# Kernel optimization log

Hardware: AMD Instinct MI355X
Metric: run time of the kernel (lower is better)

## Reference

```python
import jax, jax.numpy as jnp
import numpy as np

N_NODES = 50000
N_EDGES = 800000
IN_DIM = 512
HIDDEN = 512
NUM_HASH = 4
HASH_DIM = 128
NUM_GRAPHS = 64
NUM_CLASSES = 10


def _hash_mats(rng, num_hash, in_dim, hash_dim):
    # Each row of each hash matrix has a single +-1 entry at a random column.
    cols = rng.integers(0, hash_dim, size=(num_hash, in_dim))
    signs = (rng.integers(0, 2, size=(num_hash, in_dim)) * 2 - 1).astype(np.float32)
    W = np.zeros((num_hash, in_dim, hash_dim), dtype=np.float32)
    W[np.arange(num_hash)[:, None], np.arange(in_dim)[None, :], cols] = signs
    return jnp.asarray(W)


def setup_inputs() -> dict:
    key = jax.random.key(0)
    ks = jax.random.split(key, 10)
    rng = np.random.default_rng(0)
    x = jax.random.normal(ks[0], (N_NODES, IN_DIM), dtype=jnp.float32)
    edge_index = jax.random.randint(ks[1], (2, N_EDGES), 0, N_NODES, dtype=jnp.int64)
    batch = jnp.sort(jax.random.randint(ks[2], (N_NODES,), 0, NUM_GRAPHS, dtype=jnp.int64))
    s1 = 1.0 / np.sqrt(NUM_HASH * HASH_DIM)
    s2 = 1.0 / np.sqrt(IN_DIM)
    s3 = 1.0 / np.sqrt(HIDDEN)
    return {
        "x": x,
        "edge_index": edge_index,
        "batch": batch,
        "Hm1": _hash_mats(rng, NUM_HASH, IN_DIM, HASH_DIM),
        "Wp1": jax.random.normal(ks[3], (NUM_HASH * HASH_DIM, HIDDEN), dtype=jnp.float32) * s1,
        "Ws1": jax.random.normal(ks[4], (IN_DIM, HIDDEN), dtype=jnp.float32) * s2,
        "b1": jnp.zeros((HIDDEN,), dtype=jnp.float32),
        "Hm2": _hash_mats(rng, NUM_HASH, HIDDEN, HASH_DIM),
        "Wp2": jax.random.normal(ks[5], (NUM_HASH * HASH_DIM, HIDDEN), dtype=jnp.float32) * s1,
        "Ws2": jax.random.normal(ks[6], (HIDDEN, HIDDEN), dtype=jnp.float32) * s3,
        "b2": jnp.zeros((HIDDEN,), dtype=jnp.float32),
        "Wc": jax.random.normal(ks[7], (HIDDEN, NUM_CLASSES), dtype=jnp.float32) * s3,
        "bc": jnp.zeros((NUM_CLASSES,), dtype=jnp.float32),
    }


def _demo_layer(h, src, dst, deg, Hm, Wp, Ws, b):
    n = h.shape[0]
    # Degree-bucketed gather + mean == segment-mean over edges by source node.
    nsum = jax.ops.segment_sum(h[dst], src, num_segments=n)  # [N, D]
    agg = jnp.where(deg[:, None] > 0, nsum / jnp.maximum(deg, 1.0)[:, None], h)
    # Multi-hash matmul + concat: [N, K*HASH_DIM]
    hashed = jnp.einsum("nd,kdh->nkh", agg, Hm).reshape(n, -1)
    out = hashed @ Wp + h @ Ws + b
    return jax.nn.elu(out)  # dropout is identity in eval mode


def reference(x, edge_index, batch, Hm1, Wp1, Ws1, b1, Hm2, Wp2, Ws2, b2, Wc, bc):
    n = x.shape[0]
    src, dst = edge_index[0], edge_index[1]
    deg = jax.ops.segment_sum(jnp.ones(src.shape, x.dtype), src, num_segments=n)
    h = _demo_layer(x, src, dst, deg, Hm1, Wp1, Ws1, b1)
    h = _demo_layer(h, src, dst, deg, Hm2, Wp2, Ws2, b2)
    # global mean pool per graph
    cnt = jax.ops.segment_sum(jnp.ones((n,), h.dtype), batch, num_segments=NUM_GRAPHS)
    g = jax.ops.segment_sum(h, batch, num_segments=NUM_GRAPHS) / jnp.maximum(cnt, 1.0)[:, None]
    return g @ Wc + bc
```

## Files before the change

kernel.cpp:

```cpp
#include <hip/hip_runtime.h>
#include <hip/hip_bf16.h>
#include <math.h>

#define N_NODES_C 50000
#define N_EDGES_C 800000
#define DIM 512
#define NUM_GRAPHS_C 64
#define NUM_CLASSES_C 10

#define NROWT ((N_NODES_C + 127) / 128)
#define GEMM_BLOCKS (((NROWT * 4 + 31) / 32) * 32)

#define SCAN_BLK 1024
#define SCAN_NBLK ((N_NODES_C + SCAN_BLK - 1) / SCAN_BLK)

typedef short bf16x8 __attribute__((ext_vector_type(8)));
typedef short bf16x4 __attribute__((ext_vector_type(4)));
typedef float f32x4 __attribute__((ext_vector_type(4)));
typedef float f32x2 __attribute__((ext_vector_type(2)));
typedef unsigned u32x2 __attribute__((ext_vector_type(2)));

__device__ __forceinline__ float bf2f(short s) {
    return __uint_as_float(((unsigned)(unsigned short)s) << 16);
}
__device__ __forceinline__ short f2bf(float f) {
    unsigned u = __float_as_uint(f);
    u += 0x7FFF + ((u >> 16) & 1);
    return (short)(u >> 16);
}
__device__ __forceinline__ float eluf(float v) {
    return v > 0.0f ? v : __expf(v) - 1.0f;
}
__device__ __forceinline__ unsigned f32x4_to_fp8(float a, float b, float c, float d) {
    int w = 0;
    w = __builtin_amdgcn_cvt_pk_fp8_f32(a, b, w, false);
    w = __builtin_amdgcn_cvt_pk_fp8_f32(c, d, w, true);
    return (unsigned)w;
}
__device__ __forceinline__ void acc_fp8x8(float* acc, u32x2 w) {
    f32x2 a = __builtin_amdgcn_cvt_pk_f32_fp8((int)w[0], false);
    f32x2 b = __builtin_amdgcn_cvt_pk_f32_fp8((int)w[0], true);
    f32x2 c = __builtin_amdgcn_cvt_pk_f32_fp8((int)w[1], false);
    f32x2 d = __builtin_amdgcn_cvt_pk_f32_fp8((int)w[1], true);
    acc[0] += a[0]; acc[1] += a[1]; acc[2] += b[0]; acc[3] += b[1];
    acc[4] += c[0]; acc[5] += c[1]; acc[6] += d[0]; acc[7] += d[1];
}

__device__ __forceinline__ void gl16(const void* g, void* l) {
    __builtin_amdgcn_global_load_lds(
        (const __attribute__((address_space(1))) unsigned*)g,
        (__attribute__((address_space(3))) unsigned*)l, 16, 0, 0);
}


__global__ void k_hist(const int* __restrict__ src, int* __restrict__ cnt) {
    int e = blockIdx.x * blockDim.x + threadIdx.x;
    if (e < N_EDGES_C) atomicAdd(&cnt[src[e]], 1);
}

__global__ __launch_bounds__(1024)
void k_bsum(const int* __restrict__ cnt, int* __restrict__ bsum) {
    __shared__ int sh[1024];
    int i = blockIdx.x * 1024 + threadIdx.x;
    sh[threadIdx.x] = (i < N_NODES_C) ? cnt[i] : 0;
    __syncthreads();
    for (int ofs = 512; ofs > 0; ofs >>= 1) {
        if ((int)threadIdx.x < ofs) sh[threadIdx.x] += sh[threadIdx.x + ofs];
        __syncthreads();
    }
    if (threadIdx.x == 0) bsum[blockIdx.x] = sh[0];
}

__global__ __launch_bounds__(64)
void k_bscan(const int* __restrict__ bsum, int* __restrict__ bofs,
             int* __restrict__ start) {
    int l = threadIdx.x;
    int own = (l < SCAN_NBLK) ? bsum[l] : 0;
    int v = own;
    for (int ofs = 1; ofs < 64; ofs <<= 1) {
        int t = __shfl_up(v, ofs, 64);
        if (l >= ofs) v += t;
    }
    if (l < SCAN_NBLK) bofs[l] = v - own;
    if (l == 63) start[N_NODES_C] = v;
}

__global__ __launch_bounds__(1024)
void k_scan_apply(const int* __restrict__ cnt, const int* __restrict__ bofs,
                  int* __restrict__ start, int* __restrict__ cursor) {
    __shared__ int sh[1024];
    int i = blockIdx.x * 1024 + threadIdx.x;
    int v = (i < N_NODES_C) ? cnt[i] : 0;
    sh[threadIdx.x] = v;
    __syncthreads();
    for (int ofs = 1; ofs < 1024; ofs <<= 1) {
        int t = (threadIdx.x >= (unsigned)ofs) ? sh[threadIdx.x - ofs] : 0;
        __syncthreads();
        sh[threadIdx.x] += t;
        __syncthreads();
    }
    if (i < N_NODES_C) {
        int ex = bofs[blockIdx.x] + sh[threadIdx.x] - v;
        start[i] = ex;
        cursor[i] = ex;
    }
}

__global__ void k_fill(const int* __restrict__ src, const int* __restrict__ dst,
                       int* __restrict__ cursor, int* __restrict__ ebuf) {
    int e = blockIdx.x * blockDim.x + threadIdx.x;
    if (e < N_EDGES_C) {
        int pos = atomicAdd(&cursor[src[e]], 1);
        ebuf[pos] = dst[e];
    }
}

__global__ __launch_bounds__(1024)
void k_cnt(const int* __restrict__ batch, int* __restrict__ cnt) {
    __shared__ int h[NUM_GRAPHS_C];
    if (threadIdx.x < NUM_GRAPHS_C) h[threadIdx.x] = 0;
    __syncthreads();
    int n = blockIdx.x * blockDim.x + threadIdx.x;
    if (n < N_NODES_C) {
        int g = batch[n];
        if ((unsigned)g < NUM_GRAPHS_C) atomicAdd(&h[g], 1);
    }
    __syncthreads();
    if (threadIdx.x < NUM_GRAPHS_C && h[threadIdx.x] > 0)
        atomicAdd(&cnt[threadIdx.x], h[threadIdx.x]);
}

__global__ void k_weff(const float* __restrict__ Hm, const float* __restrict__ Wp,
                       float* __restrict__ Weff) {
    __shared__ int   scol[4];
    __shared__ float ssign[4];
    int d = blockIdx.x;
    int h = threadIdx.x;
    for (int k = 0; k < 4; ++k) {
        float v = Hm[((size_t)k * DIM + d) * 128 + h];
        if (v != 0.0f) { scol[k] = h; ssign[k] = v; }
    }
    __syncthreads();
    for (int j = threadIdx.x; j < DIM; j += 128) {
        float acc = 0.0f;
#pragma unroll
        for (int k = 0; k < 4; ++k)
            acc += ssign[k] * Wp[(size_t)(k * 128 + scol[k]) * DIM + j];
        Weff[(size_t)d * DIM + j] = acc;
    }
}

__global__ void k_prepw(const float* __restrict__ Weff, const float* __restrict__ Ws,
                        short* __restrict__ Wt) {
    int n = blockIdx.x;
    for (int k = threadIdx.x; k < 2 * DIM; k += 256) {
        float v = (k < DIM) ? Weff[(size_t)k * DIM + n] : Ws[(size_t)(k - DIM) * DIM + n];
        Wt[(size_t)n * (2 * DIM) + k] = f2bf(v);
    }
}

__global__ void k_cast(const float* __restrict__ x, short* __restrict__ xb,
                       unsigned char* __restrict__ xq) {
    int idx = blockIdx.x * blockDim.x + threadIdx.x;
    if (idx >= N_NODES_C * DIM / 8) return;
    const float* p = x + (size_t)idx * 8;
    float v[8];
    bf16x8 o;
#pragma unroll
    for (int j = 0; j < 8; ++j) { v[j] = p[j]; o[j] = f2bf(v[j]); }
    u32x2 q;
    q[0] = f32x4_to_fp8(v[0], v[1], v[2], v[3]);
    q[1] = f32x4_to_fp8(v[4], v[5], v[6], v[7]);
    *(bf16x8*)(xb + (size_t)idx * 8) = o;
    *(u32x2*)(xq + (size_t)idx * 8) = q;
}

__global__ __launch_bounds__(256)
void k_gather_8(const unsigned char* __restrict__ Hq, const int* __restrict__ start,
                const int* __restrict__ ebuf, const short* __restrict__ fb,
                short* __restrict__ outb) {
    int n = blockIdx.x * 4 + (threadIdx.x >> 6);
    int l = threadIdx.x & 63;
    if (n >= N_NODES_C) return;
    int s = start[n], e = start[n + 1];
    float acc[8] = {0, 0, 0, 0, 0, 0, 0, 0};
    int i = s;
    if (i + 4 <= e) {
        int d0 = ebuf[i], d1 = ebuf[i + 1], d2 = ebuf[i + 2], d3 = ebuf[i + 3];
        for (; i + 8 <= e; i += 4) {
            int n0 = ebuf[i + 4], n1 = ebuf[i + 5], n2 = ebuf[i + 6], n3 = ebuf[i + 7];
            u32x2 w0 = *(const u32x2*)(Hq + (size_t)d0 * DIM + l * 8);
            u32x2 w1 = *(const u32x2*)(Hq + (size_t)d1 * DIM + l * 8);
            u32x2 w2 = *(const u32x2*)(Hq + (size_t)d2 * DIM + l * 8);
            u32x2 w3 = *(const u32x2*)(Hq + (size_t)d3 * DIM + l * 8);
            acc_fp8x8(acc, w0); acc_fp8x8(acc, w1);
            acc_fp8x8(acc, w2); acc_fp8x8(acc, w3);
            d0 = n0; d1 = n1; d2 = n2; d3 = n3;
        }
        {
            u32x2 w0 = *(const u32x2*)(Hq + (size_t)d0 * DIM + l * 8);
            u32x2 w1 = *(const u32x2*)(Hq + (size_t)d1 * DIM + l * 8);
            u32x2 w2 = *(const u32x2*)(Hq + (size_t)d2 * DIM + l * 8);
            u32x2 w3 = *(const u32x2*)(Hq + (size_t)d3 * DIM + l * 8);
            acc_fp8x8(acc, w0); acc_fp8x8(acc, w1);
            acc_fp8x8(acc, w2); acc_fp8x8(acc, w3);
            i += 4;
        }
    }
    for (; i < e; ++i) {
        int d0 = ebuf[i];
        u32x2 w0 = *(const u32x2*)(Hq + (size_t)d0 * DIM + l * 8);
        acc_fp8x8(acc, w0);
    }
    bf16x8 o;
    if (e > s) {
        float inv = 1.0f / (float)(e - s);
#pragma unroll
        for (int j = 0; j < 8; ++j) o[j] = f2bf(acc[j] * inv);
    } else {
        o = *(const bf16x8*)(fb + (size_t)n * DIM + l * 8);
    }
    *(bf16x8*)(outb + (size_t)n * DIM + l * 8) = o;
}


__device__ __forceinline__ void gemm_core(const short* __restrict__ A1,
                                          const short* __restrict__ A2,
                                          const short* __restrict__ Wt,
                                          short* As, short* Bs,
                                          int row0, int col0,
                                          int wave, int lane, f32x4 (*acc)[4]) {
    const int wm = wave >> 1, wn = wave & 1;
    const int q = lane >> 4, t16 = lane & 15;
    const int rloc = wave * 32 + (lane >> 3);
    const int csrc = (lane & 7) ^ (lane >> 3);
    size_t aoff[4], boff[4];
#pragma unroll
    for (int j = 0; j < 4; ++j) {
        int grow = row0 + rloc + j * 8;
        if (grow >= N_NODES_C) grow = N_NODES_C - 1;
        aoff[j] = (size_t)grow * DIM + csrc * 8;
        boff[j] = (size_t)(col0 + rloc + j * 8) * (2 * DIM) + csrc * 8;
    }
    short* AsW = As + wave * 2048;
    short* BsW = Bs + wave * 2048;
#pragma unroll
    for (int p = 0; p < 2; ++p) {
        const short* A = p ? A2 : A1;
        const short* W = Wt + p * DIM;
        for (int kt = 0; kt < DIM; kt += 64) {
            __syncthreads();
#pragma unroll
            for (int j = 0; j < 4; ++j) {
                gl16(A + aoff[j] + kt, AsW + j * 512);
                gl16(W + boff[j] + kt, BsW + j * 512);
            }
            __syncthreads();
#pragma unroll
            for (int kh = 0; kh < 2; ++kh) {
                bf16x8 af[4], bfv[4];
#pragma unroll
                for (int mi = 0; mi < 4; ++mi) {
                    int r = wm * 64 + mi * 16 + t16;
                    int cp = (kh * 4 + q) ^ (t16 & 7);
                    af[mi] = *(const bf16x8*)(As + r * 64 + cp * 8);
                }
#pragma unroll
                for (int ni = 0; ni < 4; ++ni) {
                    int r = wn * 64 + ni * 16 + t16;
                    int cp = (kh * 4 + q) ^ (t16 & 7);
                    bfv[ni] = *(const bf16x8*)(Bs + r * 64 + cp * 8);
                }
#pragma unroll
                for (int mi = 0; mi < 4; ++mi)
#pragma unroll
                    for (int ni = 0; ni < 4; ++ni)
                        acc[mi][ni] = __builtin_amdgcn_mfma_f32_16x16x32_bf16(
                            bfv[ni], af[mi], acc[mi][ni], 0, 0, 0);
            }
        }
    }
}

__global__ __launch_bounds__(256, 4)
void k_gemm_elu_mfma(const short* __restrict__ A1, const short* __restrict__ A2,
                     const short* __restrict__ Wt, const float* __restrict__ bias,
                     short* __restrict__ C, unsigned char* __restrict__ C8) {
    __shared__ __align__(16) short As[128 * 64];
    __shared__ __align__(16) short Bs[128 * 64];
    const int L = blockIdx.x;
    const int ct = (L & 31) >> 3;
    const int rt = ((L >> 5) << 3) + (L & 7);
    if (rt >= NROWT) return;
    const int row0 = rt * 128, col0 = ct * 128;
    const int tid = threadIdx.x;
    const int lane = tid & 63, wave = tid >> 6;
    const int wm = wave >> 1, wn = wave & 1;
    const int q = lane >> 4, t16 = lane & 15;
    f32x4 acc[4][4] = {};
    gemm_core(A1, A2, Wt, As, Bs, row0, col0, wave, lane, acc);
    f32x4 bv[4];
#pragma unroll
    for (int ni = 0; ni < 4; ++ni)
        bv[ni] = *(const f32x4*)(bias + col0 + wn * 64 + ni * 16 + q * 4);
#pragma unroll
    for (int mi = 0; mi < 4; ++mi) {
        int row = row0 + wm * 64 + mi * 16 + t16;
        if (row < N_NODES_C) {
#pragma unroll
            for (int ni = 0; ni < 4; ++ni) {
                int colq = col0 + wn * 64 + ni * 16 + q * 4;
                float v0 = eluf(acc[mi][ni][0] + bv[ni][0]);
                float v1 = eluf(acc[mi][ni][1] + bv[ni][1]);
                float v2 = eluf(acc[mi][ni][2] + bv[ni][2]);
                float v3 = eluf(acc[mi][ni][3] + bv[ni][3]);
                bf16x4 ob;
                ob[0] = f2bf(v0); ob[1] = f2bf(v1);
                ob[2] = f2bf(v2); ob[3] = f2bf(v3);
                *(bf16x4*)(C + (size_t)row * DIM + colq) = ob;
                *(unsigned*)(C8 + (size_t)row * DIM + colq) =
                    f32x4_to_fp8(v0, v1, v2, v3);
            }
        }
    }
}

__global__ __launch_bounds__(256, 4)
void k_gemm_pool_mfma(const short* __restrict__ A1, const short* __restrict__ A2,
                      const short* __restrict__ Wt, const float* __restrict__ bias,
                      const int* __restrict__ batch, float* __restrict__ gsum) {
    __shared__ __align__(16) short As[128 * 64];
    __shared__ __align__(16) short Bs[128 * 64];
    __shared__ int sbatch[128];
    const int L = blockIdx.x;
    const int ct = (L & 31) >> 3;
    const int rt = ((L >> 5) << 3) + (L & 7);
    if (rt >= NROWT) return;
    const int row0 = rt * 128, col0 = ct * 128;
    const int tid = threadIdx.x;
    const int lane = tid & 63, wave = tid >> 6;
    const int wm = wave >> 1, wn = wave & 1;
    const int q = lane >> 4, t16 = lane & 15;
    if (tid < 128) {
        int rw = row0 + tid;
        sbatch[tid] = (rw < N_NODES_C) ? batch[rw] : -1;
    }
    f32x4 acc[4][4] = {};
    gemm_core(A1, A2, Wt, As, Bs, row0, col0, wave, lane, acc);
    f32x4 bv[4];
#pragma unroll
    for (int ni = 0; ni < 4; ++ni)
        bv[ni] = *(const f32x4*)(bias + col0 + wn * 64 + ni * 16 + q * 4);
    const int g0 = sbatch[wm * 64];
    const int g63 = sbatch[wm * 64 + 63];
    if (g0 == g63) {
        if (g0 >= 0) {
#pragma unroll
            for (int ni = 0; ni < 4; ++ni) {
#pragma unroll
                for (int r = 0; r < 4; ++r) {
                    float s = 0.0f;
#pragma unroll
                    for (int mi = 0; mi < 4; ++mi)
                        s += eluf(acc[mi][ni][r] + bv[ni][r]);
                    s += __shfl_xor(s, 1, 64);
                    s += __shfl_xor(s, 2, 64);
                    s += __shfl_xor(s, 4, 64);
                    s += __shfl_xor(s, 8, 64);
                    if (t16 == 0)
                        atomicAdd(&gsum[(size_t)g0 * DIM + col0 + wn * 64 +
                                        ni * 16 + q * 4 + r], s);
                }
            }
        }
    } else if (g0 >= 0) {
        int g_th[4];
#pragma unroll
        for (int mi = 0; mi < 4; ++mi) g_th[mi] = sbatch[wm * 64 + mi * 16 + t16];
        int gmx = g0;
#pragma unroll
        for (int mi = 0; mi < 4; ++mi) gmx = max(gmx, g_th[mi]);
        gmx = max(gmx, __shfl_xor(gmx, 1, 64));
        gmx = max(gmx, __shfl_xor(gmx, 2, 64));
        gmx = max(gmx, __shfl_xor(gmx, 4, 64));
        gmx = max(gmx, __shfl_xor(gmx, 8, 64));
        for (int gsel = g0; gsel <= gmx; ++gsel) {
#pragma unroll
            for (int ni = 0; ni < 4; ++ni) {
#pragma unroll
                for (int r = 0; r < 4; ++r) {
                    float s = 0.0f;
#pragma unroll
                    for (int mi = 0; mi < 4; ++mi) {
                        float v = eluf(acc[mi][ni][r] + bv[ni][r]);
                        s += (g_th[mi] == gsel) ? v : 0.0f;
                    }
                    s += __shfl_xor(s, 1, 64);
                    s += __shfl_xor(s, 2, 64);
                    s += __shfl_xor(s, 4, 64);
                    s += __shfl_xor(s, 8, 64);
                    if (t16 == 0)
                        atomicAdd(&gsum[(size_t)gsel * DIM + col0 + wn * 64 +
                                        ni * 16 + q * 4 + r], s);
                }
            }
        }
    }
}

__global__ void k_final(const float* __restrict__ gsum, const int* __restrict__ cnt,
                        const float* __restrict__ Wc, const float* __restrict__ bc,
                        float* __restrict__ out) {
    int g = blockIdx.x;
    int j = threadIdx.x;
    if (j >= NUM_CLASSES_C) return;
    int c_ = cnt[g];
    float inv = 1.0f / (float)(c_ > 1 ? c_ : 1);
    float s = 0.0f;
    for (int c = 0; c < DIM; ++c)
        s += gsum[(size_t)g * DIM + c] * Wc[(size_t)c * NUM_CLASSES_C + j];
    out[g * NUM_CLASSES_C + j] = s * inv + bc[j];
}


extern "C" void kernel_launch(void* const* d_in, const int* in_sizes, int n_in,
                              void* d_out, int out_size, void* d_ws, size_t ws_size,
                              hipStream_t stream) {
    const float* x   = (const float*)d_in[0];
    const int*   ei  = (const int*)d_in[1];
    const int*   src = ei;
    const int*   dst = ei + N_EDGES_C;
    const int* batch = (const int*)d_in[2];
    const float* Hm1 = (const float*)d_in[3];
    const float* Wp1 = (const float*)d_in[4];
    const float* Ws1 = (const float*)d_in[5];
    const float* b1  = (const float*)d_in[6];
    const float* Hm2 = (const float*)d_in[7];
    const float* Wp2 = (const float*)d_in[8];
    const float* Ws2 = (const float*)d_in[9];
    const float* b2  = (const float*)d_in[10];
    const float* Wc  = (const float*)d_in[11];
    const float* bc  = (const float*)d_in[12];
    float* out = (float*)d_out;

    char* ws = (char*)d_ws;
    size_t off = 0;
    auto alloc = [&](size_t bytes) {
        void* p = ws + off;
        off += (bytes + 255) & ~(size_t)255;
        return p;
    };
    const size_t nodeB16 = (size_t)N_NODES_C * DIM * 2;
    const size_t nodeB8  = (size_t)N_NODES_C * DIM;
    short* xb    = (short*)alloc(nodeB16);
    short* aggB  = (short*)alloc(nodeB16);
    short* hB    = (short*)alloc(nodeB16);
    unsigned char* xq = (unsigned char*)alloc(nodeB8);
    unsigned char* hq = (unsigned char*)alloc(nodeB8);
    float* Weff1 = (float*)alloc((size_t)DIM * DIM * 4);
    float* Weff2 = (float*)alloc((size_t)DIM * DIM * 4);
    short* Wt1   = (short*)alloc((size_t)DIM * 2 * DIM * 2);
    short* Wt2   = (short*)alloc((size_t)DIM * 2 * DIM * 2);
    int*   cnt_i = (int*)alloc((size_t)N_NODES_C * 4);
    int*   start = (int*)alloc((size_t)(N_NODES_C + 1) * 4);
    int*   cursor= (int*)alloc((size_t)N_NODES_C * 4);
    int*   ebuf  = (int*)alloc((size_t)N_EDGES_C * 4);
    int*   cnt   = (int*)alloc((size_t)NUM_GRAPHS_C * 4);
    float* gsum  = (float*)alloc((size_t)NUM_GRAPHS_C * DIM * 4);
    int*   bsum  = (int*)alloc((size_t)SCAN_NBLK * 4);
    int*   bofs  = (int*)alloc((size_t)SCAN_NBLK * 4);

    hipMemsetAsync(cnt_i, 0, (size_t)N_NODES_C * 4, stream);
    hipMemsetAsync(cnt, 0, (size_t)NUM_GRAPHS_C * 4, stream);
    hipMemsetAsync(gsum, 0, (size_t)NUM_GRAPHS_C * DIM * 4, stream);

    k_hist<<<(N_EDGES_C + 255) / 256, 256, 0, stream>>>(src, cnt_i);
    k_bsum<<<SCAN_NBLK, 1024, 0, stream>>>(cnt_i, bsum);
    k_bscan<<<1, 64, 0, stream>>>(bsum, bofs, start);
    k_scan_apply<<<SCAN_NBLK, 1024, 0, stream>>>(cnt_i, bofs, start, cursor);
    k_fill<<<(N_EDGES_C + 255) / 256, 256, 0, stream>>>(src, dst, cursor, ebuf);
    k_cnt<<<(N_NODES_C + 1023) / 1024, 1024, 0, stream>>>(batch, cnt);
    k_weff<<<DIM, 128, 0, stream>>>(Hm1, Wp1, Weff1);
    k_weff<<<DIM, 128, 0, stream>>>(Hm2, Wp2, Weff2);
    k_prepw<<<DIM, 256, 0, stream>>>(Weff1, Ws1, Wt1);
    k_prepw<<<DIM, 256, 0, stream>>>(Weff2, Ws2, Wt2);
    k_cast<<<(N_NODES_C * DIM / 8 + 255) / 256, 256, 0, stream>>>(x, xb, xq);

    k_gather_8<<<(N_NODES_C + 3) / 4, 256, 0, stream>>>(xq, start, ebuf, xb, aggB);
    k_gemm_elu_mfma<<<GEMM_BLOCKS, 256, 0, stream>>>(aggB, xb, Wt1, b1, hB, hq);

    k_gather_8<<<(N_NODES_C + 3) / 4, 256, 0, stream>>>(hq, start, ebuf, hB, aggB);
    k_gemm_pool_mfma<<<GEMM_BLOCKS, 256, 0, stream>>>(aggB, hB, Wt2, b2, batch, gsum);

    k_final<<<NUM_GRAPHS_C, 64, 0, stream>>>(gsum, cnt, Wc, bc, out);
}
```

Measured before the change: 606.2 us.

## Merge scan and graph-count kernels, raise GEMM occupancy, drop batch LDS staging

Folds the per-graph node count into the block-sum kernel and the single-block offset scan into the scan-apply kernel, which removes two kernel launches. Both MFMA GEMM kernels now request 5 blocks per SM instead of 4, which may force tighter register allocation. The pooling GEMM reads batch ids straight from global memory instead of staging them in shared memory. In k_scan_apply, bofs_s is written by the first wave and read after the existing __syncthreads, so ordering is kept.

Result: slower. 776.5 us (+28.1%).

```diff
diff --git a/kernel.cpp b/kernel.cpp
--- a/kernel.cpp
+++ b/kernel.cpp
@@ -59,36 +59,44 @@
 }
 
 __global__ __launch_bounds__(1024)
-void k_bsum(const int* __restrict__ cnt, int* __restrict__ bsum) {
+void k_bsum(const int* __restrict__ cnt, int* __restrict__ bsum,
+            const int* __restrict__ batch, int* __restrict__ gcnt) {
     __shared__ int sh[1024];
+    __shared__ int h[NUM_GRAPHS_C];
+    if (threadIdx.x < NUM_GRAPHS_C) h[threadIdx.x] = 0;
     int i = blockIdx.x * 1024 + threadIdx.x;
-    sh[threadIdx.x] = (i < N_NODES_C) ? cnt[i] : 0;
+    int inb = (i < N_NODES_C);
+    sh[threadIdx.x] = inb ? cnt[i] : 0;
+    if (inb) {
+        int g = batch[i];
+        if ((unsigned)g < NUM_GRAPHS_C) atomicAdd(&h[g], 1);
+    }
     __syncthreads();
     for (int ofs = 512; ofs > 0; ofs >>= 1) {
         if ((int)threadIdx.x < ofs) sh[threadIdx.x] += sh[threadIdx.x + ofs];
         __syncthreads();
     }
     if (threadIdx.x == 0) bsum[blockIdx.x] = sh[0];
-}
-
-__global__ __launch_bounds__(64)
-void k_bscan(const int* __restrict__ bsum, int* __restrict__ bofs,
-             int* __restrict__ start) {
-    int l = threadIdx.x;
-    int own = (l < SCAN_NBLK) ? bsum[l] : 0;
-    int v = own;
-    for (int ofs = 1; ofs < 64; ofs <<= 1) {
-        int t = __shfl_up(v, ofs, 64);
-        if (l >= ofs) v += t;
-    }
-    if (l < SCAN_NBLK) bofs[l] = v - own;
-    if (l == 63) start[N_NODES_C] = v;
+    if (threadIdx.x < NUM_GRAPHS_C && h[threadIdx.x] > 0)
+        atomicAdd(&gcnt[threadIdx.x], h[threadIdx.x]);
 }
 
 __global__ __launch_bounds__(1024)
-void k_scan_apply(const int* __restrict__ cnt, const int* __restrict__ bofs,
+void k_scan_apply(const int* __restrict__ cnt, const int* __restrict__ bsum,
                   int* __restrict__ start, int* __restrict__ cursor) {
     __shared__ int sh[1024];
+    __shared__ int bofs_s;
+    if (threadIdx.x < 64) {
+        int l = threadIdx.x;
+        int own = (l < SCAN_NBLK) ? bsum[l] : 0;
+        int v = own;
+        for (int ofs = 1; ofs < 64; ofs <<= 1) {
+            int t = __shfl_up(v, ofs, 64);
+            if (l >= ofs) v += t;
+        }
+        if (l == (int)blockIdx.x) bofs_s = v - own;
+        if (blockIdx.x == 0 && l == 63) start[N_NODES_C] = v;
+    }
     int i = blockIdx.x * 1024 + threadIdx.x;
     int v = (i < N_NODES_C) ? cnt[i] : 0;
     sh[threadIdx.x] = v;
@@ -100,7 +108,7 @@
         __syncthreads();
     }
     if (i < N_NODES_C) {
-        int ex = bofs[blockIdx.x] + sh[threadIdx.x] - v;
+        int ex = bofs_s + sh[threadIdx.x] - v;
         start[i] = ex;
         cursor[i] = ex;
     }
@@ -113,21 +121,6 @@
         int pos = atomicAdd(&cursor[src[e]], 1);
         ebuf[pos] = dst[e];
     }
-}
-
-__global__ __launch_bounds__(1024)
-void k_cnt(const int* __restrict__ batch, int* __restrict__ cnt) {
-    __shared__ int h[NUM_GRAPHS_C];
-    if (threadIdx.x < NUM_GRAPHS_C) h[threadIdx.x] = 0;
-    __syncthreads();
-    int n = blockIdx.x * blockDim.x + threadIdx.x;
-    if (n < N_NODES_C) {
-        int g = batch[n];
-        if ((unsigned)g < NUM_GRAPHS_C) atomicAdd(&h[g], 1);
-    }
-    __syncthreads();
-    if (threadIdx.x < NUM_GRAPHS_C && h[threadIdx.x] > 0)
-        atomicAdd(&cnt[threadIdx.x], h[threadIdx.x]);
 }
 
 __global__ void k_weff(const float* __restrict__ Hm, const float* __restrict__ Wp,
@@ -282,7 +275,7 @@
     }
 }
 
-__global__ __launch_bounds__(256, 4)
+__global__ __launch_bounds__(256, 5)
 void k_gemm_elu_mfma(const short* __restrict__ A1, const short* __restrict__ A2,
                      const short* __restrict__ Wt, const float* __restrict__ bias,
                      short* __restrict__ C, unsigned char* __restrict__ C8) {
@@ -325,13 +318,12 @@
     }
 }
 
-__global__ __launch_bounds__(256, 4)
+__global__ __launch_bounds__(256, 5)
 void k_gemm_pool_mfma(const short* __restrict__ A1, const short* __restrict__ A2,
                       const short* __restrict__ Wt, const float* __restrict__ bias,
                       const int* __restrict__ batch, float* __restrict__ gsum) {
     __shared__ __align__(16) short As[128 * 64];
     __shared__ __align__(16) short Bs[128 * 64];
-    __shared__ int sbatch[128];
     const int L = blockIdx.x;
     const int ct = (L & 31) >> 3;
     const int rt = ((L >> 5) << 3) + (L & 7);
@@ -341,18 +333,15 @@
     const int lane = tid & 63, wave = tid >> 6;
     const int wm = wave >> 1, wn = wave & 1;
     const int q = lane >> 4, t16 = lane & 15;
-    if (tid < 128) {
-        int rw = row0 + tid;
-        sbatch[tid] = (rw < N_NODES_C) ? batch[rw] : -1;
-    }
     f32x4 acc[4][4] = {};
     gemm_core(A1, A2, Wt, As, Bs, row0, col0, wave, lane, acc);
+    auto ldb = [&](int r) { return (r < N_NODES_C) ? batch[r] : -1; };
     f32x4 bv[4];
 #pragma unroll
     for (int ni = 0; ni < 4; ++ni)
         bv[ni] = *(const f32x4*)(bias + col0 + wn * 64 + ni * 16 + q * 4);
-    const int g0 = sbatch[wm * 64];
-    const int g63 = sbatch[wm * 64 + 63];
+    const int g0 = ldb(row0 + wm * 64);
+    const int g63 = ldb(row0 + wm * 64 + 63);
     if (g0 == g63) {
         if (g0 >= 0) {
 #pragma unroll
@@ -376,7 +365,7 @@
     } else if (g0 >= 0) {
         int g_th[4];
 #pragma unroll
-        for (int mi = 0; mi < 4; ++mi) g_th[mi] = sbatch[wm * 64 + mi * 16 + t16];
+        for (int mi = 0; mi < 4; ++mi) g_th[mi] = ldb(row0 + wm * 64 + mi * 16 + t16);
         int gmx = g0;
 #pragma unroll
         for (int mi = 0; mi < 4; ++mi) gmx = max(gmx, g_th[mi]);
@@ -468,18 +457,15 @@
     int*   cnt   = (int*)alloc((size_t)NUM_GRAPHS_C * 4);
     float* gsum  = (float*)alloc((size_t)NUM_GRAPHS_C * DIM * 4);
     int*   bsum  = (int*)alloc((size_t)SCAN_NBLK * 4);
-    int*   bofs  = (int*)alloc((size_t)SCAN_NBLK * 4);
 
     hipMemsetAsync(cnt_i, 0, (size_t)N_NODES_C * 4, stream);
     hipMemsetAsync(cnt, 0, (size_t)NUM_GRAPHS_C * 4, stream);
     hipMemsetAsync(gsum, 0, (size_t)NUM_GRAPHS_C * DIM * 4, stream);
 
     k_hist<<<(N_EDGES_C + 255) / 256, 256, 0, stream>>>(src, cnt_i);
-    k_bsum<<<SCAN_NBLK, 1024, 0, stream>>>(cnt_i, bsum);
-    k_bscan<<<1, 64, 0, stream>>>(bsum, bofs, start);
-    k_scan_apply<<<SCAN_NBLK, 1024, 0, stream>>>(cnt_i, bofs, start, cursor);
+    k_bsum<<<SCAN_NBLK, 1024, 0, stream>>>(cnt_i, bsum, batch, cnt);
+    k_scan_apply<<<SCAN_NBLK, 1024, 0, stream>>>(cnt_i, bsum, start, cursor);
     k_fill<<<(N_EDGES_C + 255) / 256, 256, 0, stream>>>(src, dst, cursor, ebuf);
-    k_cnt<<<(N_NODES_C + 1023) / 1024, 1024, 0, stream>>>(batch, cnt);
     k_weff<<<DIM, 128, 0, stream>>>(Hm1, Wp1, Weff1);
     k_weff<<<DIM, 128, 0, stream>>>(Hm2, Wp2, Weff2);
     k_prepw<<<DIM, 256, 0, stream>>>(Weff1, Ws1, Wt1);
```
